# Kernel optimization log

Measured on AMD Instinct MI355X. Metric: run time of the kernel, lower is better.

The kernel has to match this reference:

```python
import jax, jax.numpy as jnp
import numpy as np
import math

B, T, H, N2 = 4, 64, 1280, 32  # batch, seq, d_model, d_state//2
D_IN = 224 * 224 * 3
R_HID, N_CLS = 64, 60


def setup_inputs() -> dict:
    key = jax.random.key(0)
    ks = jax.random.split(key, 12)
    x = jax.random.normal(ks[0], (B, T, 224, 224, 3), jnp.float32)
    # bottleneck Linear(D_IN, H)
    Wb = jax.random.normal(ks[1], (H, D_IN), jnp.float32) / math.sqrt(D_IN)
    bb = jnp.zeros((H,), jnp.float32)
    # S4D kernel params (is_real=True path)
    log_dt_min, log_dt_max = math.log(1e-3), math.log(1e-1)
    log_dt = jax.random.uniform(ks[2], (H,), jnp.float32, log_dt_min, log_dt_max)
    C = jax.random.normal(ks[3], (H, N2), jnp.float32)
    log_A_real = jnp.log(0.5 * jnp.ones((H, N2), jnp.float32))
    D = jax.random.normal(ks[4], (H,), jnp.float32)
    # output_linear: Conv1d(H, 2H, 1) + GLU(dim=-2)
    Wc = jax.random.normal(ks[5], (2 * H, H), jnp.float32) / math.sqrt(H)
    bc = jnp.zeros((2 * H,), jnp.float32)
    # readout MLP
    W1 = jax.random.normal(ks[6], (R_HID, H), jnp.float32) / math.sqrt(H)
    b1 = jnp.zeros((R_HID,), jnp.float32)
    W2 = jax.random.normal(ks[7], (N_CLS, R_HID), jnp.float32) / math.sqrt(R_HID)
    b2 = jnp.zeros((N_CLS,), jnp.float32)
    return {"x": x, "Wb": Wb, "bb": bb, "log_dt": log_dt, "C": C,
            "log_A_real": log_A_real, "D": D, "Wc": Wc, "bc": bc,
            "W1": W1, "b1": b1, "W2": W2, "b2": b2}


def _s4d_kernel(log_dt, log_A_real, C, L):
    # is_real=True: A real negative diagonal, C real. K: (H, L)
    dt = jnp.exp(log_dt)                      # (H,)
    A = -jnp.exp(log_A_real)                  # (H, N2)
    dtA = A * dt[:, None]                     # (H, N2)
    Cb = C * (jnp.exp(dtA) - 1.0) / A         # (H, N2)
    vand = jnp.exp(dtA[:, :, None] * jnp.arange(L, dtype=dtA.dtype))  # (H, N2, L)
    return 2.0 * jnp.einsum("hn,hnl->hl", Cb, vand)


def reference(x, Wb, bb, log_dt, C, log_A_real, D, Wc, bc, W1, b1, W2, b2):
    b, t = x.shape[0], x.shape[1]
    xf = x.reshape(b, t, -1)                  # (B, T, D_IN)
    u = xf @ Wb.T + bb                        # (B, T, H) bottleneck
    ut = jnp.swapaxes(u, -1, -2)              # (B, H, L) transposed=False path
    L = t
    k = _s4d_kernel(log_dt, log_A_real, C, L)  # (H, L)
    # FFT convolution (length 2L, causal crop)
    k_f = jnp.fft.rfft(k, n=2 * L)            # (H, L+1)
    u_f = jnp.fft.rfft(ut, n=2 * L)           # (B, H, L+1)
    y = jnp.fft.irfft(u_f * k_f, n=2 * L)[..., :L]
    y = y + ut * D[:, None]                   # skip connection
    y = jax.nn.gelu(y, approximate=False)     # torch GELU (exact)
    # 1x1 conv to 2H then GLU along channel dim
    z = jnp.einsum("oh,bhl->bol", Wc, y) + bc[None, :, None]
    a, g = jnp.split(z, 2, axis=1)
    y = a * jax.nn.sigmoid(g)                 # (B, H, L)
    y = jnp.swapaxes(y, -1, -2)               # (B, L, H)
    last = y[:, -1, :]                        # (B, H)
    h = jax.nn.relu(last @ W1.T + b1)
    return h @ W2.T + b2                      # (B, N_CLS)
```

## Files before the change

kernel.cpp:

```cpp
#include <hip/hip_runtime.h>
#include <hip/hip_bf16.h>
#include <math.h>

typedef __attribute__((ext_vector_type(8))) short short8;
typedef __attribute__((ext_vector_type(4))) float f32x4;
typedef __attribute__((ext_vector_type(4))) unsigned int u32x4;

#define KDIM 150528
#define KDIMB ((long)KDIM * 4)
#define NT_TILES 10
#define KCHUNKS 24
#define STEPS 196
#define BK 32
#define HDIM 1280
#define MDIM 256
#define PSTRIDE (MDIM * HDIM)
#define ABYTES 32768
#define BUFB 49152

__device__ __forceinline__ unsigned int pk2(float a, float b) {
  unsigned int r;
  asm("v_cvt_pk_bf16_f32 %0, %1, %2" : "=v"(r) : "v"(a), "v"(b));
  return r;
}

__device__ __forceinline__ void gload16(const void* g, const char* l) {
  __builtin_amdgcn_global_load_lds(
      (const __attribute__((address_space(1))) unsigned int*)g,
      (__attribute__((address_space(3))) unsigned int*)l, 16, 0, 0);
}

__device__ __forceinline__ short8 frag(const char* base, int row, int cb) {
  const int sw = (row & 7) << 4;
  const f32x4 lo = *(const f32x4*)(base + row * 128 + (cb ^ sw));
  const f32x4 hi = *(const f32x4*)(base + row * 128 + ((cb + 16) ^ sw));
  union { u32x4 u; short8 s; } c;
  c.u = (u32x4){pk2(lo.x, lo.y), pk2(lo.z, lo.w), pk2(hi.x, hi.y), pk2(hi.z, hi.w)};
  return c.s;
}

__global__ __launch_bounds__(512, 2) void k_gemm(
    const float* __restrict__ X, const float* __restrict__ W,
    float* __restrict__ P) {
  extern __shared__ char smem[];
  const int swz = (blockIdx.x & 7) * 30 + (blockIdx.x >> 3);
  const int kc = swz / 10;
  const int nt = swz % 10;
  const long k0b = (long)kc * (BK * STEPS) * 4;

  const int tid = threadIdx.x;
  const int lane = tid & 63;
  const int wv = tid >> 6;
  const int wm = wv >> 1, wn = wv & 1;
  const int frow = lane & 15;
  const int cbase = (lane >> 4) << 5;

  const int srow = tid >> 3;
  const int perm = ((tid & 7) ^ (srow & 7)) << 4;
  const char* xbase = (const char*)X + (long)srow * KDIMB + k0b + perm;
  const char* wbase = (const char*)W + (long)(nt * 128 + srow) * KDIMB + k0b + perm;

  f32x4 acc[4][4];
#pragma unroll
  for (int i = 0; i < 4; ++i)
#pragma unroll
    for (int j = 0; j < 4; ++j) acc[i][j] = (f32x4){0.f, 0.f, 0.f, 0.f};

#define STAGE(buf, t)                                                         \
  {                                                                           \
    const long ko = (long)(t) * (BK * 4);                                     \
    _Pragma("unroll") for (int q = 0; q < 4; ++q)                             \
        gload16(xbase + (long)q * 64 * KDIMB + ko,                            \
                (buf) + q * 8192 + wv * 1024);                                \
    _Pragma("unroll") for (int q = 0; q < 2; ++q)                             \
        gload16(wbase + (long)q * 64 * KDIMB + ko,                            \
                (buf) + ABYTES + q * 8192 + wv * 1024);                       \
  }

#define COMPUTE(buf)                                                          \
  {                                                                           \
    const char* A_ = (buf);                                                   \
    const char* B_ = (buf) + ABYTES;                                          \
    short8 fa[4], fb[4];                                                      \
    _Pragma("unroll") for (int i = 0; i < 4; ++i)                             \
        fa[i] = frag(A_, wm * 64 + i * 16 + frow, cbase);                     \
    _Pragma("unroll") for (int j = 0; j < 4; ++j)                             \
        fb[j] = frag(B_, wn * 64 + j * 16 + frow, cbase);                     \
    _Pragma("unroll") for (int i = 0; i < 4; ++i)                             \
        _Pragma("unroll") for (int j = 0; j < 4; ++j)                         \
            acc[i][j] = __builtin_amdgcn_mfma_f32_16x16x32_bf16(              \
                fa[i], fb[j], acc[i][j], 0, 0, 0);                            \
  }

  char* b_cur = smem;
  char* b_nxt = smem + BUFB;
  char* b_stg = smem + 2 * BUFB;

  STAGE(b_cur, 0);
  STAGE(b_nxt, 1);

  for (int t = 0; t < STEPS - 1; ++t) {
    asm volatile("s_waitcnt vmcnt(6)" ::: "memory");
    __builtin_amdgcn_s_barrier();
    __builtin_amdgcn_sched_barrier(0);
    if (t + 2 < STEPS) STAGE(b_stg, t + 2);
    COMPUTE(b_cur);
    char* tmp = b_cur; b_cur = b_nxt; b_nxt = b_stg; b_stg = tmp;
  }
  asm volatile("s_waitcnt vmcnt(0)" ::: "memory");
  __builtin_amdgcn_s_barrier();
  __builtin_amdgcn_sched_barrier(0);
  COMPUTE(b_cur);

#undef STAGE
#undef COMPUTE

  float* Pc = P + (long)kc * PSTRIDE + nt * 128;
  const int rb = wm * 64 + ((lane >> 4) << 2);
  const int cb = wn * 64 + frow;
#pragma unroll
  for (int i = 0; i < 4; ++i)
#pragma unroll
    for (int j = 0; j < 4; ++j) {
      const int col = cb + j * 16;
#pragma unroll
      for (int r = 0; r < 4; ++r)
        Pc[(long)(rb + i * 16 + r) * HDIM + col] = acc[i][j][r];
    }
}

__global__ __launch_bounds__(256) void k_s4d(
    const float* __restrict__ log_dt, const float* __restrict__ lar,
    const float* __restrict__ C, float* __restrict__ ktab) {
  const int idx = blockIdx.x * 256 + threadIdx.x;
  const int h = idx >> 6, l = idx & 63;
  const float dt = expf(log_dt[h]);
  const float fl = (float)l;
  float acc = 0.f;
#pragma unroll 4
  for (int n = 0; n < 32; ++n) {
    const float A = -expf(lar[h * 32 + n]);
    const float dtA = A * dt;
    const float Cb = C[h * 32 + n] * expm1f(dtA) / A;
    acc += Cb * expf(dtA * fl);
  }
  ktab[idx] = 2.f * acc;
}

__global__ __launch_bounds__(256) void k_red(
    const float* __restrict__ P, const float* __restrict__ bb,
    float* __restrict__ U) {
  const int idx = blockIdx.x * 256 + threadIdx.x;
  float s = bb[idx % HDIM];
#pragma unroll
  for (int c = 0; c < KCHUNKS; ++c) s += P[(long)c * PSTRIDE + idx];
  U[idx] = s;
}

__global__ __launch_bounds__(256) void k_conv(
    const float* __restrict__ U, const float* __restrict__ ktab,
    const float* __restrict__ Dv, float* __restrict__ y63) {
  __shared__ float kt[64 * 65];
  const int t = threadIdx.x;
  const int hw = blockIdx.x * 64;
  for (int i = t; i < 4096; i += 256)
    kt[(i >> 6) * 65 + (i & 63)] = ktab[(hw + (i >> 6)) * 64 + (i & 63)];
  __syncthreads();
  const int hl = t & 63, b = t >> 6;
  const int h = hw + hl;
  float y = 0.f;
  for (int m = 0; m < 64; ++m)
    y += U[(long)(b * 64 + m) * HDIM + h] * kt[hl * 65 + (63 - m)];
  y += Dv[h] * U[(long)(b * 64 + 63) * HDIM + h];
  y63[b * HDIM + h] = 0.5f * y * (1.f + erff(y * 0.70710678118654752f));
}

__global__ __launch_bounds__(64) void k_gate(
    const float* __restrict__ y63, const float* __restrict__ Wc,
    const float* __restrict__ bc, float* __restrict__ lastv) {
  const int r = blockIdx.x;
  const int l = threadIdx.x;
  const float* wa = Wc + (long)r * HDIM;
  const float* wg = Wc + (long)(HDIM + r) * HDIM;
  float sa[4] = {0.f, 0.f, 0.f, 0.f}, sg[4] = {0.f, 0.f, 0.f, 0.f};
#pragma unroll
  for (int seg = 0; seg < 5; ++seg) {
    const int j = seg * 256 + l * 4;
    const f32x4 a4 = *(const f32x4*)(wa + j);
    const f32x4 g4 = *(const f32x4*)(wg + j);
#pragma unroll
    for (int b = 0; b < 4; ++b) {
      const f32x4 yv = *(const f32x4*)(y63 + b * HDIM + j);
      sa[b] += a4.x * yv.x + a4.y * yv.y + a4.z * yv.z + a4.w * yv.w;
      sg[b] += g4.x * yv.x + g4.y * yv.y + g4.z * yv.z + g4.w * yv.w;
    }
  }
#pragma unroll
  for (int off = 32; off; off >>= 1)
#pragma unroll
    for (int b = 0; b < 4; ++b) {
      sa[b] += __shfl_down(sa[b], off);
      sg[b] += __shfl_down(sg[b], off);
    }
  if (l == 0) {
    const float ba = bc[r], bg = bc[HDIM + r];
#pragma unroll
    for (int b = 0; b < 4; ++b) {
      const float za = ba + sa[b], zg = bg + sg[b];
      lastv[b * HDIM + r] = za / (1.f + expf(-zg));
    }
  }
}

__global__ __launch_bounds__(64) void k_head(
    const float* __restrict__ lastv, const float* __restrict__ W1,
    const float* __restrict__ b1, const float* __restrict__ W2,
    const float* __restrict__ b2, float* __restrict__ out) {
  __shared__ float ll[HDIM];
  __shared__ float h1[64];
  const int b = blockIdx.x, t = threadIdx.x;
  for (int i = t; i < HDIM; i += 64) ll[i] = lastv[b * HDIM + i];
  __syncthreads();
  {
    const float* w = W1 + t * HDIM;
    float s = b1[t];
    for (int j = 0; j < HDIM; j += 4) {
      const f32x4 wv = *(const f32x4*)(w + j);
      s += wv.x * ll[j] + wv.y * ll[j + 1] + wv.z * ll[j + 2] + wv.w * ll[j + 3];
    }
    h1[t] = fmaxf(s, 0.f);
  }
  __syncthreads();
  if (t < 60) {
    const float* w = W2 + t * 64;
    float o = b2[t];
#pragma unroll
    for (int r = 0; r < 64; ++r) o += w[r] * h1[r];
    out[b * 60 + t] = o;
  }
}

extern "C" void kernel_launch(void* const* d_in, const int* in_sizes, int n_in,
                              void* d_out, int out_size, void* d_ws, size_t ws_size,
                              hipStream_t stream) {
  const float* x   = (const float*)d_in[0];
  const float* Wb  = (const float*)d_in[1];
  const float* bb  = (const float*)d_in[2];
  const float* ldt = (const float*)d_in[3];
  const float* C   = (const float*)d_in[4];
  const float* lar = (const float*)d_in[5];
  const float* Dv  = (const float*)d_in[6];
  const float* Wc  = (const float*)d_in[7];
  const float* bc  = (const float*)d_in[8];
  const float* W1  = (const float*)d_in[9];
  const float* b1  = (const float*)d_in[10];
  const float* W2  = (const float*)d_in[11];
  const float* b2  = (const float*)d_in[12];
  float* out = (float*)d_out;

  float* P     = (float*)d_ws;
  float* ktab  = P + (long)KCHUNKS * PSTRIDE;
  float* U     = ktab + HDIM * 64;
  float* y63   = U + PSTRIDE;
  float* lastv = y63 + 4 * HDIM;

  (void)hipFuncSetAttribute(reinterpret_cast<const void*>(k_gemm),
                            hipFuncAttributeMaxDynamicSharedMemorySize,
                            3 * BUFB);

  k_s4d<<<320, 256, 0, stream>>>(ldt, lar, C, ktab);
  k_gemm<<<NT_TILES * KCHUNKS, 512, 3 * BUFB, stream>>>(x, Wb, P);
  k_red<<<PSTRIDE / 256, 256, 0, stream>>>(P, bb, U);
  k_conv<<<20, 256, 0, stream>>>(U, ktab, Dv, y63);
  k_gate<<<HDIM, 64, 0, stream>>>(y63, Wc, bc, lastv);
  k_head<<<4, 64, 0, stream>>>(lastv, W1, b1, W2, b2, out);
}
```

Measured before the change: 296.7 us.

## Stage GEMM tiles through registers with bf16 conversion before LDS write

Replaces the direct global-to-LDS fp32 loads with register-staged loads that convert to bf16 once and store packed bf16 into LDS, halving LDS footprint and removing per-fragment conversion in the compute loop. The pipeline becomes double-buffered in LDS with two register sets prefetching tiles ahead, and weight loads use nontemporal hints. This trades higher register pressure and VALU conversion on the load path for less LDS traffic and fewer repeated conversions across waves.

```diff
diff --git a/kernel.cpp b/kernel.cpp
--- a/kernel.cpp
+++ b/kernel.cpp
@@ -7,7 +7,6 @@
 typedef __attribute__((ext_vector_type(4))) unsigned int u32x4;
 
 #define KDIM 150528
-#define KDIMB ((long)KDIM * 4)
 #define NT_TILES 10
 #define KCHUNKS 24
 #define STEPS 196
@@ -15,28 +14,16 @@
 #define HDIM 1280
 #define MDIM 256
 #define PSTRIDE (MDIM * HDIM)
-#define ABYTES 32768
-#define BUFB 49152
+#define ABB 16384
+#define BUFB 24576
 
 __device__ __forceinline__ unsigned int pk2(float a, float b) {
   unsigned int r;
   asm("v_cvt_pk_bf16_f32 %0, %1, %2" : "=v"(r) : "v"(a), "v"(b));
   return r;
 }
-
-__device__ __forceinline__ void gload16(const void* g, const char* l) {
-  __builtin_amdgcn_global_load_lds(
-      (const __attribute__((address_space(1))) unsigned int*)g,
-      (__attribute__((address_space(3))) unsigned int*)l, 16, 0, 0);
-}
-
-__device__ __forceinline__ short8 frag(const char* base, int row, int cb) {
-  const int sw = (row & 7) << 4;
-  const f32x4 lo = *(const f32x4*)(base + row * 128 + (cb ^ sw));
-  const f32x4 hi = *(const f32x4*)(base + row * 128 + ((cb + 16) ^ sw));
-  union { u32x4 u; short8 s; } c;
-  c.u = (u32x4){pk2(lo.x, lo.y), pk2(lo.z, lo.w), pk2(hi.x, hi.y), pk2(hi.z, hi.w)};
-  return c.s;
+__device__ __forceinline__ u32x4 pk8(f32x4 a, f32x4 b) {
+  return (u32x4){pk2(a.x, a.y), pk2(a.z, a.w), pk2(b.x, b.y), pk2(b.z, b.w)};
 }
 
 __global__ __launch_bounds__(512, 2) void k_gemm(
@@ -46,19 +33,24 @@
   const int swz = (blockIdx.x & 7) * 30 + (blockIdx.x >> 3);
   const int kc = swz / 10;
   const int nt = swz % 10;
-  const long k0b = (long)kc * (BK * STEPS) * 4;
+  const long k0 = (long)kc * (BK * STEPS);
 
   const int tid = threadIdx.x;
   const int lane = tid & 63;
   const int wv = tid >> 6;
   const int wm = wv >> 1, wn = wv & 1;
   const int frow = lane & 15;
-  const int cbase = (lane >> 4) << 5;
-
-  const int srow = tid >> 3;
-  const int perm = ((tid & 7) ^ (srow & 7)) << 4;
-  const char* xbase = (const char*)X + (long)srow * KDIMB + k0b + perm;
-  const char* wbase = (const char*)W + (long)(nt * 128 + srow) * KDIMB + k0b + perm;
+  const int fslot = lane >> 4;
+
+  const int r0 = tid >> 2;
+  const int s = tid & 3;
+  const float* xA0 = X + (long)r0 * KDIM + k0 + s * 8;
+  const float* xA1 = X + (long)(r0 + 128) * KDIM + k0 + s * 8;
+  const float* wB0 = W + (long)(nt * 128 + r0) * KDIM + k0 + s * 8;
+  const int ssw = (s ^ ((r0 >> 1) & 3)) << 4;
+  const int aoff0 = r0 * 64 + ssw;
+  const int aoff1 = (r0 + 128) * 64 + ssw;
+  const int boff = ABB + r0 * 64 + ssw;
 
   f32x4 acc[4][4];
 #pragma unroll
@@ -66,54 +58,76 @@
 #pragma unroll
     for (int j = 0; j < 4; ++j) acc[i][j] = (f32x4){0.f, 0.f, 0.f, 0.f};
 
-#define STAGE(buf, t)                                                         \
+  f32x4 A0a, A0b, A1a, A1b, B0a, B0b;
+  f32x4 C0a, C0b, C1a, C1b, D0a, D0b;
+
+#define LOADS(p0, p1, p2, p3, p4, p5, t)                                      \
   {                                                                           \
-    const long ko = (long)(t) * (BK * 4);                                     \
-    _Pragma("unroll") for (int q = 0; q < 4; ++q)                             \
-        gload16(xbase + (long)q * 64 * KDIMB + ko,                            \
-                (buf) + q * 8192 + wv * 1024);                                \
-    _Pragma("unroll") for (int q = 0; q < 2; ++q)                             \
-        gload16(wbase + (long)q * 64 * KDIMB + ko,                            \
-                (buf) + ABYTES + q * 8192 + wv * 1024);                       \
-  }
-
+    const long off = (long)(t)*BK;                                            \
+    p0 = *(const f32x4*)(xA0 + off);                                          \
+    p1 = *(const f32x4*)(xA0 + off + 4);                                      \
+    p2 = *(const f32x4*)(xA1 + off);                                          \
+    p3 = *(const f32x4*)(xA1 + off + 4);                                      \
+    p4 = __builtin_nontemporal_load((const f32x4*)(wB0 + off));               \
+    p5 = __builtin_nontemporal_load((const f32x4*)(wB0 + off + 4));           \
+  }
+#define CVTWRITE(buf, p0, p1, p2, p3, p4, p5)                                 \
+  {                                                                           \
+    *(u32x4*)((buf) + aoff0) = pk8(p0, p1);                                   \
+    *(u32x4*)((buf) + aoff1) = pk8(p2, p3);                                   \
+    *(u32x4*)((buf) + boff) = pk8(p4, p5);                                    \
+  }
 #define COMPUTE(buf)                                                          \
   {                                                                           \
-    const char* A_ = (buf);                                                   \
-    const char* B_ = (buf) + ABYTES;                                          \
+    const char* L_ = (buf);                                                   \
     short8 fa[4], fb[4];                                                      \
-    _Pragma("unroll") for (int i = 0; i < 4; ++i)                             \
-        fa[i] = frag(A_, wm * 64 + i * 16 + frow, cbase);                     \
-    _Pragma("unroll") for (int j = 0; j < 4; ++j)                             \
-        fb[j] = frag(B_, wn * 64 + j * 16 + frow, cbase);                     \
+    _Pragma("unroll") for (int i = 0; i < 4; ++i) {                           \
+      const int R = wm * 64 + i * 16 + frow;                                  \
+      fa[i] = *(const short8*)(L_ + R * 64 + ((fslot ^ ((R >> 1) & 3)) << 4)); \
+    }                                                                         \
+    _Pragma("unroll") for (int j = 0; j < 4; ++j) {                           \
+      const int R = wn * 64 + j * 16 + frow;                                  \
+      fb[j] = *(const short8*)(L_ + ABB + R * 64 +                            \
+                               ((fslot ^ ((R >> 1) & 3)) << 4));              \
+    }                                                                         \
     _Pragma("unroll") for (int i = 0; i < 4; ++i)                             \
         _Pragma("unroll") for (int j = 0; j < 4; ++j)                         \
             acc[i][j] = __builtin_amdgcn_mfma_f32_16x16x32_bf16(              \
                 fa[i], fb[j], acc[i][j], 0, 0, 0);                            \
   }
-
-  char* b_cur = smem;
-  char* b_nxt = smem + BUFB;
-  char* b_stg = smem + 2 * BUFB;
-
-  STAGE(b_cur, 0);
-  STAGE(b_nxt, 1);
-
-  for (int t = 0; t < STEPS - 1; ++t) {
-    asm volatile("s_waitcnt vmcnt(6)" ::: "memory");
-    __builtin_amdgcn_s_barrier();
+#define STEPBAR()                                                             \
+  asm volatile("s_waitcnt lgkmcnt(0)" ::: "memory");                          \
+  __builtin_amdgcn_s_barrier();                                               \
+  __builtin_amdgcn_sched_barrier(0);
+
+  char* buf0 = smem;
+  char* buf1 = smem + BUFB;
+
+  LOADS(A0a, A0b, A1a, A1b, B0a, B0b, 0);
+  LOADS(C0a, C0b, C1a, C1b, D0a, D0b, 1);
+  CVTWRITE(buf0, A0a, A0b, A1a, A1b, B0a, B0b);
+  LOADS(A0a, A0b, A1a, A1b, B0a, B0b, 2);
+  STEPBAR();
+
+  for (int t = 0; t < STEPS; t += 2) {
+    CVTWRITE(buf1, C0a, C0b, C1a, C1b, D0a, D0b);
+    if (t + 3 < STEPS) LOADS(C0a, C0b, C1a, C1b, D0a, D0b, t + 3);
     __builtin_amdgcn_sched_barrier(0);
-    if (t + 2 < STEPS) STAGE(b_stg, t + 2);
-    COMPUTE(b_cur);
-    char* tmp = b_cur; b_cur = b_nxt; b_nxt = b_stg; b_stg = tmp;
-  }
-  asm volatile("s_waitcnt vmcnt(0)" ::: "memory");
-  __builtin_amdgcn_s_barrier();
-  __builtin_amdgcn_sched_barrier(0);
-  COMPUTE(b_cur);
-
-#undef STAGE
+    COMPUTE(buf0);
+    STEPBAR();
+    if (t + 2 < STEPS) {
+      CVTWRITE(buf0, A0a, A0b, A1a, A1b, B0a, B0b);
+      if (t + 4 < STEPS) LOADS(A0a, A0b, A1a, A1b, B0a, B0b, t + 4);
+    }
+    __builtin_amdgcn_sched_barrier(0);
+    COMPUTE(buf1);
+    STEPBAR();
+  }
+
+#undef LOADS
+#undef CVTWRITE
 #undef COMPUTE
+#undef STEPBAR
 
   float* Pc = P + (long)kc * PSTRIDE + nt * 128;
   const int rb = wm * 64 + ((lane >> 4) << 2);
@@ -266,10 +280,10 @@
 
   (void)hipFuncSetAttribute(reinterpret_cast<const void*>(k_gemm),
                             hipFuncAttributeMaxDynamicSharedMemorySize,
-                            3 * BUFB);
+                            2 * BUFB);
 
   k_s4d<<<320, 256, 0, stream>>>(ldt, lar, C, ktab);
-  k_gemm<<<NT_TILES * KCHUNKS, 512, 3 * BUFB, stream>>>(x, Wb, P);
+  k_gemm<<<NT_TILES * KCHUNKS, 512, 2 * BUFB, stream>>>(x, Wb, P);
   k_red<<<PSTRIDE / 256, 256, 0, stream>>>(P, bb, U);
   k_conv<<<20, 256, 0, stream>>>(U, ktab, Dv, y63);
   k_gate<<<HDIM, 64, 0, stream>>>(y63, Wc, bc, lastv);
```

New measurement: 327.6 us. 1.1x slower.

## Warp-specialize GEMM: producer waves convert fp32 to bf16 in LDS, consumers run MFMA

Applied to the files above, without the earlier changes.

The bottleneck GEMM is rewritten with warp specialization. Four producer waves load fp32 tiles into registers, convert them to bf16 once and write them into a triple-buffered LDS layout with padded rows. Four consumer waves read ready bf16 fragments and issue MFMAs at raised priority. The tile shrinks from 256x128 to 128x128 with an extra M-tile grid dimension, so the grid doubles and LDS per block drops. This removes the repeated per-wave fp32-to-bf16 conversion and the double-size fp32 LDS traffic, at the cost of re-reading the W tiles for each M-tile and having only half the waves doing MFMA work.

```diff
diff --git a/kernel.cpp b/kernel.cpp
--- a/kernel.cpp
+++ b/kernel.cpp
@@ -7,126 +7,130 @@
 typedef __attribute__((ext_vector_type(4))) unsigned int u32x4;
 
 #define KDIM 150528
-#define KDIMB ((long)KDIM * 4)
 #define NT_TILES 10
+#define MT_TILES 2
 #define KCHUNKS 24
+#define CHUNK_K 6272
 #define STEPS 196
 #define BK 32
 #define HDIM 1280
 #define MDIM 256
 #define PSTRIDE (MDIM * HDIM)
-#define ABYTES 32768
-#define BUFB 49152
+#define AREG 10240
+#define BUFB 20480
 
 __device__ __forceinline__ unsigned int pk2(float a, float b) {
   unsigned int r;
   asm("v_cvt_pk_bf16_f32 %0, %1, %2" : "=v"(r) : "v"(a), "v"(b));
   return r;
 }
-
-__device__ __forceinline__ void gload16(const void* g, const char* l) {
-  __builtin_amdgcn_global_load_lds(
-      (const __attribute__((address_space(1))) unsigned int*)g,
-      (__attribute__((address_space(3))) unsigned int*)l, 16, 0, 0);
-}
-
-__device__ __forceinline__ short8 frag(const char* base, int row, int cb) {
-  const int sw = (row & 7) << 4;
-  const f32x4 lo = *(const f32x4*)(base + row * 128 + (cb ^ sw));
-  const f32x4 hi = *(const f32x4*)(base + row * 128 + ((cb + 16) ^ sw));
-  union { u32x4 u; short8 s; } c;
-  c.u = (u32x4){pk2(lo.x, lo.y), pk2(lo.z, lo.w), pk2(hi.x, hi.y), pk2(hi.z, hi.w)};
-  return c.s;
+__device__ __forceinline__ u32x4 pk8(f32x4 a, f32x4 b) {
+  return (u32x4){pk2(a.x, a.y), pk2(a.z, a.w), pk2(b.x, b.y), pk2(b.z, b.w)};
 }
 
 __global__ __launch_bounds__(512, 2) void k_gemm(
     const float* __restrict__ X, const float* __restrict__ W,
     float* __restrict__ P) {
   extern __shared__ char smem[];
-  const int swz = (blockIdx.x & 7) * 30 + (blockIdx.x >> 3);
-  const int kc = swz / 10;
-  const int nt = swz % 10;
-  const long k0b = (long)kc * (BK * STEPS) * 4;
+  const int swz = (blockIdx.x & 7) * 60 + (blockIdx.x >> 3);
+  const int kc = swz / 20;
+  const int rem = swz % 20;
+  const int nt = rem >> 1;
+  const int mt = rem & 1;
+  const long k0 = (long)kc * CHUNK_K;
 
   const int tid = threadIdx.x;
   const int lane = tid & 63;
   const int wv = tid >> 6;
-  const int wm = wv >> 1, wn = wv & 1;
-  const int frow = lane & 15;
-  const int cbase = (lane >> 4) << 5;
-
-  const int srow = tid >> 3;
-  const int perm = ((tid & 7) ^ (srow & 7)) << 4;
-  const char* xbase = (const char*)X + (long)srow * KDIMB + k0b + perm;
-  const char* wbase = (const char*)W + (long)(nt * 128 + srow) * KDIMB + k0b + perm;
-
-  f32x4 acc[4][4];
-#pragma unroll
-  for (int i = 0; i < 4; ++i)
-#pragma unroll
-    for (int j = 0; j < 4; ++j) acc[i][j] = (f32x4){0.f, 0.f, 0.f, 0.f};
-
-#define STAGE(buf, t)                                                         \
+
+  if (wv >= 4) {
+    const int r = (wv - 4) * 32 + (lane >> 1);
+    const int h = lane & 1;
+    const float* ga = X + (long)(mt * 128 + r) * KDIM + k0 + h * 16;
+    const float* gb = W + (long)(nt * 128 + r) * KDIM + k0 + h * 16;
+    const int wa = r * 80 + h * 32;
+    const int wb = AREG + r * 80 + h * 32;
+    f32x4 a0, a1, a2, a3, b0, b1, b2, b3;
+#define LOADP(t)                                                              \
   {                                                                           \
-    const long ko = (long)(t) * (BK * 4);                                     \
-    _Pragma("unroll") for (int q = 0; q < 4; ++q)                             \
-        gload16(xbase + (long)q * 64 * KDIMB + ko,                            \
-                (buf) + q * 8192 + wv * 1024);                                \
-    _Pragma("unroll") for (int q = 0; q < 2; ++q)                             \
-        gload16(wbase + (long)q * 64 * KDIMB + ko,                            \
-                (buf) + ABYTES + q * 8192 + wv * 1024);                       \
-  }
-
-#define COMPUTE(buf)                                                          \
+    const long o = (long)(t) * BK;                                            \
+    a0 = *(const f32x4*)(ga + o);      a1 = *(const f32x4*)(ga + o + 4);      \
+    a2 = *(const f32x4*)(ga + o + 8);  a3 = *(const f32x4*)(ga + o + 12);     \
+    b0 = *(const f32x4*)(gb + o);      b1 = *(const f32x4*)(gb + o + 4);      \
+    b2 = *(const f32x4*)(gb + o + 8);  b3 = *(const f32x4*)(gb + o + 12);     \
+  }
+#define CVTW(buf)                                                             \
   {                                                                           \
-    const char* A_ = (buf);                                                   \
-    const char* B_ = (buf) + ABYTES;                                          \
-    short8 fa[4], fb[4];                                                      \
-    _Pragma("unroll") for (int i = 0; i < 4; ++i)                             \
-        fa[i] = frag(A_, wm * 64 + i * 16 + frow, cbase);                     \
-    _Pragma("unroll") for (int j = 0; j < 4; ++j)                             \
-        fb[j] = frag(B_, wn * 64 + j * 16 + frow, cbase);                     \
-    _Pragma("unroll") for (int i = 0; i < 4; ++i)                             \
-        _Pragma("unroll") for (int j = 0; j < 4; ++j)                         \
-            acc[i][j] = __builtin_amdgcn_mfma_f32_16x16x32_bf16(              \
-                fa[i], fb[j], acc[i][j], 0, 0, 0);                            \
-  }
-
-  char* b_cur = smem;
-  char* b_nxt = smem + BUFB;
-  char* b_stg = smem + 2 * BUFB;
-
-  STAGE(b_cur, 0);
-  STAGE(b_nxt, 1);
-
-  for (int t = 0; t < STEPS - 1; ++t) {
-    asm volatile("s_waitcnt vmcnt(6)" ::: "memory");
+    *(u32x4*)((buf) + wa) = pk8(a0, a1);                                      \
+    *(u32x4*)((buf) + wa + 16) = pk8(a2, a3);                                 \
+    *(u32x4*)((buf) + wb) = pk8(b0, b1);                                      \
+    *(u32x4*)((buf) + wb + 16) = pk8(b2, b3);                                 \
+  }
+    LOADP(0);
+    CVTW(smem);
+    LOADP(1);
+    asm volatile("s_waitcnt lgkmcnt(0)" ::: "memory");
     __builtin_amdgcn_s_barrier();
-    __builtin_amdgcn_sched_barrier(0);
-    if (t + 2 < STEPS) STAGE(b_stg, t + 2);
-    COMPUTE(b_cur);
-    char* tmp = b_cur; b_cur = b_nxt; b_nxt = b_stg; b_stg = tmp;
-  }
-  asm volatile("s_waitcnt vmcnt(0)" ::: "memory");
-  __builtin_amdgcn_s_barrier();
-  __builtin_amdgcn_sched_barrier(0);
-  COMPUTE(b_cur);
-
-#undef STAGE
-#undef COMPUTE
-
-  float* Pc = P + (long)kc * PSTRIDE + nt * 128;
-  const int rb = wm * 64 + ((lane >> 4) << 2);
-  const int cb = wn * 64 + frow;
-#pragma unroll
-  for (int i = 0; i < 4; ++i)
-#pragma unroll
-    for (int j = 0; j < 4; ++j) {
-      const int col = cb + j * 16;
-#pragma unroll
-      for (int r = 0; r < 4; ++r)
-        Pc[(long)(rb + i * 16 + r) * HDIM + col] = acc[i][j][r];
-    }
+    int nb = 1;
+    for (int t = 0; t < STEPS; ++t) {
+      if (t + 1 < STEPS) CVTW(smem + nb * BUFB);
+      if (t + 2 < STEPS) LOADP(t + 2);
+      __builtin_amdgcn_sched_barrier(0);
+      asm volatile("s_waitcnt lgkmcnt(0)" ::: "memory");
+      __builtin_amdgcn_s_barrier();
+      nb = (nb == 2) ? 0 : nb + 1;
+    }
+#undef LOADP
+#undef CVTW
+  } else {
+    const int wm = wv >> 1, wn = wv & 1;
+    const int frow = lane & 15;
+    const int fsl = (lane >> 4) << 4;
+    int aoff[4], boff[4];
+#pragma unroll
+    for (int i = 0; i < 4; ++i) {
+      aoff[i] = (wm * 64 + i * 16 + frow) * 80 + fsl;
+      boff[i] = AREG + (wn * 64 + i * 16 + frow) * 80 + fsl;
+    }
+    f32x4 acc[4][4];
+#pragma unroll
+    for (int i = 0; i < 4; ++i)
+#pragma unroll
+      for (int j = 0; j < 4; ++j) acc[i][j] = (f32x4){0.f, 0.f, 0.f, 0.f};
+
+    __builtin_amdgcn_s_barrier();
+    int cb = 0;
+    for (int t = 0; t < STEPS; ++t) {
+      const char* bf = smem + cb * BUFB;
+      __builtin_amdgcn_s_setprio(1);
+      short8 fa[4];
+#pragma unroll
+      for (int i = 0; i < 4; ++i) fa[i] = *(const short8*)(bf + aoff[i]);
+#pragma unroll
+      for (int j = 0; j < 4; ++j) {
+        const short8 fb = *(const short8*)(bf + boff[j]);
+#pragma unroll
+        for (int i = 0; i < 4; ++i)
+          acc[i][j] = __builtin_amdgcn_mfma_f32_16x16x32_bf16(fa[i], fb,
+                                                              acc[i][j], 0, 0, 0);
+      }
+      __builtin_amdgcn_s_setprio(0);
+      __builtin_amdgcn_s_barrier();
+      cb = (cb == 2) ? 0 : cb + 1;
+    }
+    float* Pc = P + (long)kc * PSTRIDE + (long)mt * 128 * HDIM + nt * 128;
+    const int rb = wm * 64 + ((lane >> 4) << 2);
+    const int cbase = wn * 64 + frow;
+#pragma unroll
+    for (int i = 0; i < 4; ++i)
+#pragma unroll
+      for (int j = 0; j < 4; ++j) {
+        const int col = cbase + j * 16;
+#pragma unroll
+        for (int r = 0; r < 4; ++r)
+          Pc[(long)(rb + i * 16 + r) * HDIM + col] = acc[i][j][r];
+      }
+  }
 }
 
 __global__ __launch_bounds__(256) void k_s4d(
@@ -269,7 +273,7 @@
                             3 * BUFB);
 
   k_s4d<<<320, 256, 0, stream>>>(ldt, lar, C, ktab);
-  k_gemm<<<NT_TILES * KCHUNKS, 512, 3 * BUFB, stream>>>(x, Wb, P);
+  k_gemm<<<NT_TILES * MT_TILES * KCHUNKS, 512, 3 * BUFB, stream>>>(x, Wb, P);
   k_red<<<PSTRIDE / 256, 256, 0, stream>>>(P, bb, U);
   k_conv<<<20, 256, 0, stream>>>(U, ktab, Dv, y63);
   k_gate<<<HDIM, 64, 0, stream>>>(y63, Wc, bc, lastv);
```

Result: slower. 369.0 us (+24.4%).
